# Optimization experiments

Measured on AMD Instinct MI355X. Metric: run time of the kernel, lower is better.

## Reference

```python
import jax, jax.numpy as jnp
import numpy as np

HIDDEN = 1024
INTER = 4096
NUM_EXPERTS = 8
TOP_K = 2


def setup_inputs() -> dict:
    key = jax.random.key(0)
    ks = jax.random.split(key, 6)
    B, S = 4, 2048
    hidden_states = jax.random.normal(ks[0], (B, S, HIDDEN), dtype=jnp.float32)
    scale = 0.02
    # nn.Linear stores weight as [out, in]; y = x @ W.T + b
    gate_w = jax.random.normal(ks[1], (NUM_EXPERTS, HIDDEN), dtype=jnp.float32) * scale
    W1 = jax.random.normal(ks[2], (NUM_EXPERTS, INTER, HIDDEN), dtype=jnp.float32) * scale
    b1 = jax.random.normal(ks[3], (NUM_EXPERTS, INTER), dtype=jnp.float32) * scale
    W2 = jax.random.normal(ks[4], (NUM_EXPERTS, HIDDEN, INTER), dtype=jnp.float32) * scale
    b2 = jax.random.normal(ks[5], (NUM_EXPERTS, HIDDEN), dtype=jnp.float32) * scale
    return {"hidden_states": hidden_states, "gate_w": gate_w,
            "W1": W1, "b1": b1, "W2": W2, "b2": b2}


def reference(hidden_states, gate_w, W1, b1, W2, b2):
    B, S, H = hidden_states.shape
    x = hidden_states.reshape(-1, H)                      # [T, H]
    # Gating: top-k logits -> softmax over the k selected experts only
    gate_logits = x @ gate_w.T                            # [T, E]
    top_vals, top_idx = jax.lax.top_k(gate_logits, TOP_K) # [T, K]
    weights = jax.nn.softmax(top_vals, axis=-1)           # [T, K]
    # Per-token combine weight for each expert (0 if not selected)
    one_hot = jax.nn.one_hot(top_idx, NUM_EXPERTS, dtype=x.dtype)  # [T, K, E]
    combine = jnp.einsum("tk,tke->te", weights, one_hot)           # [T, E]
    # Expert MLPs: fixed small loop over experts (structurally distinct params)
    out = jnp.zeros_like(x)
    for e in range(NUM_EXPERTS):
        h = jax.nn.gelu(x @ W1[e].T + b1[e], approximate=False)  # [T, INTER]
        y = h @ W2[e].T + b2[e]                                   # [T, H]
        out = out + combine[:, e:e + 1] * y
    return out.reshape(B, S, H)
```

## Files before the change

### kernel.cpp

```cpp
#include <hip/hip_runtime.h>
#include <hip/hip_bf16.h>
#include <stdint.h>

#define HID 1024
#define INTER_ 4096
#define NE 8
#define NTOK 8192
#define NPAIR (NTOK * 2)
#define MAXT 72

using f32x4 = __attribute__((ext_vector_type(4))) float;
using bf16x8 = __attribute__((ext_vector_type(8))) __bf16;
using ushort8v = __attribute__((ext_vector_type(8))) unsigned short;

__device__ __forceinline__ unsigned short f2b(float f) {
  unsigned int u = __float_as_uint(f);
  u += 0x7fffu + ((u >> 16) & 1u);
  return (unsigned short)(u >> 16);
}
__device__ __forceinline__ float b2f(unsigned short u) {
  return __uint_as_float((unsigned int)u << 16);
}

__device__ __forceinline__ float gelu_f(float v) {
  float z = fabsf(v) * 0.70710678118654752f;
  float t = __builtin_amdgcn_rcpf(1.f + 0.3275911f * z);
  float p = t * (0.254829592f +
            t * (-0.284496736f +
            t * (1.421413741f +
            t * (-1.453152027f + t * 1.061405429f))));
  float er = 1.f - p * __expf(-z * z);
  er = copysignf(er, v);
  return 0.5f * v * (1.f + er);
}

#define GLD_LDS(gp, lp)                                                        \
  __builtin_amdgcn_global_load_lds(                                            \
      (const __attribute__((address_space(1))) unsigned int*)(const void*)(gp),\
      (__attribute__((address_space(3))) unsigned int*)(void*)(lp), 16, 0, 0)

#define WAITV(N) asm volatile("s_waitcnt vmcnt(" #N ")" ::: "memory")

__global__ __launch_bounds__(256) void gate_kernel(
    const float* __restrict__ x, const float* __restrict__ gw,
    int* __restrict__ topi, float* __restrict__ topw,
    unsigned short* __restrict__ xb)
{
  int gwave = (blockIdx.x * 256 + threadIdx.x) >> 6;
  int lane = threadIdx.x & 63;
  if (gwave >= NTOK) return;
  const float* xr = x + (size_t)gwave * HID;
  unsigned short* xo = xb + (size_t)gwave * HID;
  float acc[NE];
#pragma unroll
  for (int e = 0; e < NE; ++e) acc[e] = 0.f;
#pragma unroll
  for (int q = 0; q < 4; ++q) {
    float4 v = *reinterpret_cast<const float4*>(xr + q * 256 + lane * 4);
    ushort4 uv;
    uv.x = f2b(v.x); uv.y = f2b(v.y); uv.z = f2b(v.z); uv.w = f2b(v.w);
    *reinterpret_cast<ushort4*>(xo + q * 256 + lane * 4) = uv;
#pragma unroll
    for (int e = 0; e < NE; ++e) {
      float4 wv = *reinterpret_cast<const float4*>(gw + e * HID + q * 256 + lane * 4);
      acc[e] += v.x * wv.x + v.y * wv.y + v.z * wv.z + v.w * wv.w;
    }
  }
#pragma unroll
  for (int e = 0; e < NE; ++e) {
#pragma unroll
    for (int off = 32; off > 0; off >>= 1) acc[e] += __shfl_xor(acc[e], off);
  }
  if (lane == 0) {
    float v0 = -1e30f; int i0 = 0;
#pragma unroll
    for (int e = 0; e < NE; ++e) if (acc[e] > v0) { v0 = acc[e]; i0 = e; }
    float v1 = -1e30f; int i1 = 0;
#pragma unroll
    for (int e = 0; e < NE; ++e) if (e != i0 && acc[e] > v1) { v1 = acc[e]; i1 = e; }
    float e1 = __expf(v1 - v0);
    float s = 1.f + e1;
    topi[gwave * 2] = i0; topi[gwave * 2 + 1] = i1;
    topw[gwave * 2] = 1.f / s; topw[gwave * 2 + 1] = e1 / s;
  }
}

__global__ __launch_bounds__(256) void hist_kernel(const int* __restrict__ topi,
                                                   int* __restrict__ bcnt)
{
  int tid = threadIdx.x, blk = blockIdx.x;
  int t = blk * 256 + tid;
  int e0 = topi[t * 2], e1 = topi[t * 2 + 1];
  int w = tid >> 6, lane = tid & 63;
  __shared__ int wcnt[4][NE];
#pragma unroll
  for (int e = 0; e < NE; ++e) {
    unsigned long long m0 = __ballot(e0 == e);
    unsigned long long m1 = __ballot(e1 == e);
    if (lane == 0) wcnt[w][e] = __popcll(m0) + __popcll(m1);
  }
  __syncthreads();
  if (tid < NE) {
    int s = 0;
#pragma unroll
    for (int w2 = 0; w2 < 4; ++w2) s += wcnt[w2][tid];
    bcnt[blk * NE + tid] = s;
  }
}

__global__ void scan2_kernel(const int* __restrict__ bcnt, int* __restrict__ offs,
                             int* __restrict__ tile_e, int* __restrict__ tile_m,
                             int* __restrict__ ntile, int* __restrict__ gbase)
{
  __shared__ int cnts[NE];
  __shared__ int soffs[NE];
  int tid = threadIdx.x;
  if (tid < NE) {
    int s = 0;
#pragma unroll
    for (int b = 0; b < 32; ++b) s += bcnt[b * NE + tid];
    cnts[tid] = s;
  }
  __syncthreads();
  if (tid == 0) {
    int o = 0, tt = 0;
    for (int e = 0; e < NE; ++e) {
      offs[e] = o; soffs[e] = o;
      int c = cnts[e];
      for (int m = 0; m < c; m += 256) { tile_e[tt] = e; tile_m[tt] = m; ++tt; }
      o += c;
    }
    offs[NE] = o;
    *ntile = tt;
  }
  __syncthreads();
  if (tid < 32 * NE) {
    int b = tid >> 3, e = tid & 7;
    int g = soffs[e];
    for (int b2 = 0; b2 < b; ++b2) g += bcnt[b2 * NE + e];
    gbase[b * NE + e] = g;
  }
}

__global__ __launch_bounds__(256) void scatter2_kernel(
    const int* __restrict__ topi, const float* __restrict__ topw,
    const int* __restrict__ gbase,
    int* __restrict__ toklist, float* __restrict__ wlist, int* __restrict__ pos)
{
  int tid = threadIdx.x, blk = blockIdx.x;
  int t = blk * 256 + tid;
  int e0 = topi[t * 2], e1 = topi[t * 2 + 1];
  float w0 = topw[t * 2], w1 = topw[t * 2 + 1];
  int w = tid >> 6, lane = tid & 63;
  unsigned long long lt = (1ull << lane) - 1ull;
  unsigned long long le = lt | (1ull << lane);
  __shared__ int wcnt[4][NE];
  __shared__ int wbase[4][NE];
  int r0 = 0, r1 = 0;
#pragma unroll
  for (int e = 0; e < NE; ++e) {
    unsigned long long m0 = __ballot(e0 == e);
    unsigned long long m1 = __ballot(e1 == e);
    if (lane == 0) wcnt[w][e] = __popcll(m0) + __popcll(m1);
    if (e0 == e) r0 = __popcll(m0 & lt) + __popcll(m1 & lt);
    if (e1 == e) r1 = __popcll(m0 & le) + __popcll(m1 & lt);
  }
  __syncthreads();
  if (tid < 4 * NE) {
    int w2 = tid >> 3, e = tid & 7;
    int b = gbase[blk * NE + e];
    for (int w3 = 0; w3 < w2; ++w3) b += wcnt[w3][e];
    wbase[w2][e] = b;
  }
  __syncthreads();
  int P0 = wbase[w][e0] + r0;
  int P1 = wbase[w][e1] + r1;
  toklist[P0] = t; wlist[P0] = w0; pos[t * 2] = P0;
  toklist[P1] = t; wlist[P1] = w1; pos[t * 2 + 1] = P1;
}

__global__ __launch_bounds__(256) void cvtw_kernel(
    const float* __restrict__ W1, const float* __restrict__ W2,
    unsigned short* __restrict__ w1b, unsigned short* __restrict__ w2b, int n8)
{
  int half = gridDim.x >> 1;
  const float* src = (blockIdx.x < half) ? W1 : W2;
  unsigned short* dst = (blockIdx.x < half) ? w1b : w2b;
  int b0 = (blockIdx.x < half) ? blockIdx.x : blockIdx.x - half;
  int stride = half * 256;
  for (int i = b0 * 256 + threadIdx.x; i < n8; i += stride) {
    const float4* s = reinterpret_cast<const float4*>(src) + (size_t)i * 2;
    float4 a = s[0], b = s[1];
    ushort8v u;
    u[0] = f2b(a.x); u[1] = f2b(a.y); u[2] = f2b(a.z); u[3] = f2b(a.w);
    u[4] = f2b(b.x); u[5] = f2b(b.y); u[6] = f2b(b.z); u[7] = f2b(b.w);
    reinterpret_cast<ushort8v*>(dst)[i] = u;
  }
}


__global__ __launch_bounds__(512, 2) void gemm1_kernel(
    const unsigned short* __restrict__ xb, const unsigned short* __restrict__ w1b,
    const float* __restrict__ b1,
    const int* __restrict__ toklist, const int* __restrict__ offs,
    const int* __restrict__ tile_e, const int* __restrict__ tile_m,
    const int* __restrict__ ntile,
    unsigned short* __restrict__ hb)
{
  const int t = blockIdx.y;
  if (t >= *ntile) return;
  const int e = tile_e[t];
  const int m0 = tile_m[t];
  const int base = offs[e];
  const int cnt = offs[e + 1] - base;
  const int n0 = blockIdx.x * 256;

  __shared__ __align__(16) unsigned short As[4][256 * 32];
  __shared__ __align__(16) unsigned short Bs[4][256 * 32];

  const int tid = threadIdx.x;
  const int lane = tid & 63;
  const int w = tid >> 6;
  const int wr = w >> 2, wc = w & 3;

  const int r0 = tid >> 2;
  const int sl = tid & 3;
  const int scg = sl ^ ((r0 >> 1) & 3);
  const unsigned short* gA[2];
  const unsigned short* gB[2];
#pragma unroll
  for (int g = 0; g < 2; ++g) {
    int row = g * 128 + r0;
    int mrow = m0 + row; if (mrow >= cnt) mrow = cnt - 1;
    int tk = toklist[base + mrow];
    gA[g] = xb + (size_t)tk * HID + scg * 8;
    gB[g] = w1b + ((size_t)e * INTER_ + n0 + row) * HID + scg * 8;
  }

  int raq[8], rbq[4];
#pragma unroll
  for (int i = 0; i < 8; ++i) {
    int rA = wr * 128 + i * 16 + (lane & 15);
    raq[i] = rA * 32 + (((lane >> 4) ^ ((rA >> 1) & 3)) * 8);
  }
#pragma unroll
  for (int j = 0; j < 4; ++j) {
    int rB = wc * 64 + j * 16 + (lane & 15);
    rbq[j] = rB * 32 + (((lane >> 4) ^ ((rB >> 1) & 3)) * 8);
  }

  f32x4 acc[8][4];
#pragma unroll
  for (int i = 0; i < 8; ++i)
#pragma unroll
    for (int j = 0; j < 4; ++j) acc[i][j] = (f32x4){0.f, 0.f, 0.f, 0.f};

  auto stage = [&](int s) {
    const int kof = s * 32;
    unsigned short* Ad = &As[s & 3][0];
    unsigned short* Bd = &Bs[s & 3][0];
#pragma unroll
    for (int g = 0; g < 2; ++g) {
      GLD_LDS(gA[g] + kof, Ad + g * 4096 + tid * 8);
      GLD_LDS(gB[g] + kof, Bd + g * 4096 + tid * 8);
    }
  };
  auto compute = [&](int s) {
    const unsigned short* Ab = &As[s & 3][0];
    const unsigned short* Bb = &Bs[s & 3][0];
    bf16x8 bfr[4];
#pragma unroll
    for (int j = 0; j < 4; ++j) bfr[j] = *reinterpret_cast<const bf16x8*>(Bb + rbq[j]);
#pragma unroll
    for (int i = 0; i < 8; ++i) {
      bf16x8 af = *reinterpret_cast<const bf16x8*>(Ab + raq[i]);
#pragma unroll
      for (int j = 0; j < 4; ++j)
        acc[i][j] = __builtin_amdgcn_mfma_f32_16x16x32_bf16(af, bfr[j], acc[i][j], 0, 0, 0);
    }
  };

  const int NS = HID / 32;
  stage(0); stage(1); stage(2);
#pragma unroll 4
  for (int s = 0; s < NS - 3; ++s) {
    WAITV(8);
    __builtin_amdgcn_s_barrier();
    stage(s + 3);
    compute(s);
  }
  WAITV(8); __builtin_amdgcn_s_barrier(); compute(NS - 3);
  WAITV(4); __builtin_amdgcn_s_barrier(); compute(NS - 2);
  WAITV(0); __builtin_amdgcn_s_barrier(); compute(NS - 1);

  float bias[4];
  const int colb = n0 + wc * 64 + (lane & 15);
#pragma unroll
  for (int j = 0; j < 4; ++j) bias[j] = b1[(size_t)e * INTER_ + colb + j * 16];
#pragma unroll
  for (int i = 0; i < 8; ++i) {
    int mbase = m0 + wr * 128 + i * 16 + (lane >> 4) * 4;
#pragma unroll
    for (int r = 0; r < 4; ++r) {
      int m = mbase + r;
      if (m < cnt) {
        unsigned short* hrow = hb + (size_t)(base + m) * INTER_ + colb;
#pragma unroll
        for (int j = 0; j < 4; ++j)
          hrow[j * 16] = f2b(gelu_f(acc[i][j][r] + bias[j]));
      }
    }
  }
}

__global__ __launch_bounds__(512, 2) void gemm2_kernel(
    const unsigned short* __restrict__ hb, const unsigned short* __restrict__ w2b,
    const int* __restrict__ offs,
    const int* __restrict__ tile_e, const int* __restrict__ tile_m,
    const int* __restrict__ ntile,
    unsigned short* __restrict__ part)
{
  const int t = blockIdx.y;
  if (t >= *ntile) return;
  const int e = tile_e[t];
  const int m0 = tile_m[t];
  const int base = offs[e];
  const int cnt = offs[e + 1] - base;
  const int n0 = blockIdx.x * 256;
  const int kbase = blockIdx.z * (INTER_ / 2);

  __shared__ __align__(16) unsigned short As[4][256 * 32];
  __shared__ __align__(16) unsigned short Bs[4][256 * 32];

  const int tid = threadIdx.x;
  const int lane = tid & 63;
  const int w = tid >> 6;
  const int wr = w >> 2, wc = w & 3;

  const int r0 = tid >> 2;
  const int sl = tid & 3;
  const int scg = sl ^ ((r0 >> 1) & 3);
  const unsigned short* gA[2];
  const unsigned short* gB[2];
#pragma unroll
  for (int g = 0; g < 2; ++g) {
    int row = g * 128 + r0;
    int mrow = m0 + row; if (mrow >= cnt) mrow = cnt - 1;
    gA[g] = hb + (size_t)(base + mrow) * INTER_ + kbase + scg * 8;
    gB[g] = w2b + ((size_t)e * HID + n0 + row) * INTER_ + kbase + scg * 8;
  }

  int raq[8], rbq[4];
#pragma unroll
  for (int i = 0; i < 8; ++i) {
    int rA = wr * 128 + i * 16 + (lane & 15);
    raq[i] = rA * 32 + (((lane >> 4) ^ ((rA >> 1) & 3)) * 8);
  }
#pragma unroll
  for (int j = 0; j < 4; ++j) {
    int rB = wc * 64 + j * 16 + (lane & 15);
    rbq[j] = rB * 32 + (((lane >> 4) ^ ((rB >> 1) & 3)) * 8);
  }

  f32x4 acc[8][4];
#pragma unroll
  for (int i = 0; i < 8; ++i)
#pragma unroll
    for (int j = 0; j < 4; ++j) acc[i][j] = (f32x4){0.f, 0.f, 0.f, 0.f};

  auto stage = [&](int s) {
    const int kof = s * 32;
    unsigned short* Ad = &As[s & 3][0];
    unsigned short* Bd = &Bs[s & 3][0];
#pragma unroll
    for (int g = 0; g < 2; ++g) {
      GLD_LDS(gA[g] + kof, Ad + g * 4096 + tid * 8);
      GLD_LDS(gB[g] + kof, Bd + g * 4096 + tid * 8);
    }
  };
  auto compute = [&](int s) {
    const unsigned short* Ab = &As[s & 3][0];
    const unsigned short* Bb = &Bs[s & 3][0];
    bf16x8 bfr[4];
#pragma unroll
    for (int j = 0; j < 4; ++j) bfr[j] = *reinterpret_cast<const bf16x8*>(Bb + rbq[j]);
#pragma unroll
    for (int i = 0; i < 8; ++i) {
      bf16x8 af = *reinterpret_cast<const bf16x8*>(Ab + raq[i]);
#pragma unroll
      for (int j = 0; j < 4; ++j)
        acc[i][j] = __builtin_amdgcn_mfma_f32_16x16x32_bf16(af, bfr[j], acc[i][j], 0, 0, 0);
    }
  };

  const int NS = (INTER_ / 2) / 32;
  stage(0); stage(1); stage(2);
#pragma unroll 4
  for (int s = 0; s < NS - 3; ++s) {
    WAITV(8);
    __builtin_amdgcn_s_barrier();
    stage(s + 3);
    compute(s);
  }
  WAITV(8); __builtin_amdgcn_s_barrier(); compute(NS - 3);
  WAITV(4); __builtin_amdgcn_s_barrier(); compute(NS - 2);
  WAITV(0); __builtin_amdgcn_s_barrier(); compute(NS - 1);

  const int colb = n0 + wc * 64 + (lane & 15);
  unsigned short* pbase = part + (size_t)blockIdx.z * NPAIR * HID;
#pragma unroll
  for (int i = 0; i < 8; ++i) {
    int mbase = m0 + wr * 128 + i * 16 + (lane >> 4) * 4;
#pragma unroll
    for (int r = 0; r < 4; ++r) {
      int m = mbase + r;
      if (m < cnt) {
        unsigned short* prow = pbase + (size_t)(base + m) * HID + colb;
#pragma unroll
        for (int j = 0; j < 4; ++j)
          prow[j * 16] = f2b(acc[i][j][r]);
      }
    }
  }
}

__global__ __launch_bounds__(256) void combine_kernel(
    const unsigned short* __restrict__ part, const float* __restrict__ b2,
    const int* __restrict__ topi, const float* __restrict__ topw,
    const int* __restrict__ pos, float* __restrict__ out)
{
  int t = blockIdx.x * 4 + (threadIdx.x >> 6);
  int lane = threadIdx.x & 63;
  int c0 = lane * 16;
  float o[16];
#pragma unroll
  for (int c = 0; c < 16; ++c) o[c] = 0.f;
#pragma unroll
  for (int k = 0; k < 2; ++k) {
    int p = pos[t * 2 + k];
    int e = topi[t * 2 + k];
    float wk = topw[t * 2 + k];
    const unsigned short* rp0 = part + (size_t)p * HID + c0;
    const unsigned short* rp1 = part + ((size_t)NPAIR + p) * HID + c0;
    const float* bb = b2 + (size_t)e * HID + c0;
#pragma unroll
    for (int v = 0; v < 2; ++v) {
      ushort8v a = *reinterpret_cast<const ushort8v*>(rp0 + v * 8);
      ushort8v b = *reinterpret_cast<const ushort8v*>(rp1 + v * 8);
      float4 bb0 = *reinterpret_cast<const float4*>(bb + v * 8);
      float4 bb1 = *reinterpret_cast<const float4*>(bb + v * 8 + 4);
      o[v * 8 + 0] += wk * (b2f(a[0]) + b2f(b[0]) + bb0.x);
      o[v * 8 + 1] += wk * (b2f(a[1]) + b2f(b[1]) + bb0.y);
      o[v * 8 + 2] += wk * (b2f(a[2]) + b2f(b[2]) + bb0.z);
      o[v * 8 + 3] += wk * (b2f(a[3]) + b2f(b[3]) + bb0.w);
      o[v * 8 + 4] += wk * (b2f(a[4]) + b2f(b[4]) + bb1.x);
      o[v * 8 + 5] += wk * (b2f(a[5]) + b2f(b[5]) + bb1.y);
      o[v * 8 + 6] += wk * (b2f(a[6]) + b2f(b[6]) + bb1.z);
      o[v * 8 + 7] += wk * (b2f(a[7]) + b2f(b[7]) + bb1.w);
    }
  }
  float4* op = reinterpret_cast<float4*>(out + (size_t)t * HID + c0);
#pragma unroll
  for (int v = 0; v < 4; ++v)
    op[v] = make_float4(o[v * 4], o[v * 4 + 1], o[v * 4 + 2], o[v * 4 + 3]);
}

extern "C" void kernel_launch(void* const* d_in, const int* in_sizes, int n_in,
                              void* d_out, int out_size, void* d_ws, size_t ws_size,
                              hipStream_t stream) {
  const float* x  = (const float*)d_in[0];
  const float* gw = (const float*)d_in[1];
  const float* W1 = (const float*)d_in[2];
  const float* b1 = (const float*)d_in[3];
  const float* W2 = (const float*)d_in[4];
  const float* b2 = (const float*)d_in[5];
  float* out = (float*)d_out;

  char* ws = (char*)d_ws;
  size_t off = 0;
  auto alloc = [&](size_t bytes) -> void* {
    void* p = ws + off;
    off += (bytes + 255) & ~(size_t)255;
    return p;
  };
  unsigned short* hb   = (unsigned short*)alloc((size_t)NPAIR * INTER_ * 2);
  unsigned short* xb   = (unsigned short*)alloc((size_t)NTOK * HID * 2);
  unsigned short* w1b  = (unsigned short*)alloc((size_t)NE * INTER_ * HID * 2);
  unsigned short* w2b  = (unsigned short*)alloc((size_t)NE * HID * INTER_ * 2);
  unsigned short* part = (unsigned short*)alloc((size_t)2 * NPAIR * HID * 2);
  int*   toklist = (int*)alloc(NPAIR * 4);
  float* wlist   = (float*)alloc(NPAIR * 4);
  int*   topi    = (int*)alloc(NTOK * 2 * 4);
  float* topw    = (float*)alloc(NTOK * 2 * 4);
  int*   pos     = (int*)alloc(NTOK * 2 * 4);
  int*   bcnt    = (int*)alloc(32 * NE * 4);
  int*   gbase   = (int*)alloc(32 * NE * 4);
  int*   offs    = (int*)alloc(64);
  int*   tile_e  = (int*)alloc(MAXT * 4);
  int*   tile_m  = (int*)alloc(MAXT * 4);
  int*   ntile   = (int*)alloc(64);

  gate_kernel<<<NTOK / 4, 256, 0, stream>>>(x, gw, topi, topw, xb);
  hist_kernel<<<32, 256, 0, stream>>>(topi, bcnt);
  scan2_kernel<<<1, 256, 0, stream>>>(bcnt, offs, tile_e, tile_m, ntile, gbase);
  scatter2_kernel<<<32, 256, 0, stream>>>(topi, topw, gbase, toklist, wlist, pos);
  cvtw_kernel<<<4096, 256, 0, stream>>>(W1, W2, w1b, w2b, NE * INTER_ * HID / 8);
  gemm1_kernel<<<dim3(INTER_ / 256, MAXT), 512, 0, stream>>>(
      xb, w1b, b1, toklist, offs, tile_e, tile_m, ntile, hb);
  gemm2_kernel<<<dim3(HID / 256, MAXT, 2), 512, 0, stream>>>(
      hb, w2b, offs, tile_e, tile_m, ntile, part);
  combine_kernel<<<NTOK / 4, 256, 0, stream>>>(part, b2, topi, topw, pos, out);
}
```

Before: 548.4 us.

## Drop split-K in second expert GEMM and batch LDS fragment loads with MFMA priority

The second GEMM no longer splits the K dimension across two z-blocks. Each block now covers the full INTER reduction and writes a single partial buffer, so the combine kernel reads one bf16 row instead of two and the extra partial rounding goes away. In both GEMMs the compute step now loads A fragments in two batches of four, waits on LDS, and issues the MFMAs under raised wave priority with scheduling barriers. The cost is that gemm2 launches half as many blocks, which can lower occupancy when few tiles are active, and the explicit lgkmcnt waits may serialize LDS reads against MFMA work.

```diff
diff --git a/kernel.cpp b/kernel.cpp
--- a/kernel.cpp
+++ b/kernel.cpp
@@ -40,6 +40,8 @@
       (__attribute__((address_space(3))) unsigned int*)(void*)(lp), 16, 0, 0)
 
 #define WAITV(N) asm volatile("s_waitcnt vmcnt(" #N ")" ::: "memory")
+#define WAITL0   asm volatile("s_waitcnt lgkmcnt(0)" ::: "memory")
+#define SBAR     __builtin_amdgcn_sched_barrier(0)
 
 __global__ __launch_bounds__(256) void gate_kernel(
     const float* __restrict__ x, const float* __restrict__ gw,
@@ -268,16 +270,32 @@
   auto compute = [&](int s) {
     const unsigned short* Ab = &As[s & 3][0];
     const unsigned short* Bb = &Bs[s & 3][0];
-    bf16x8 bfr[4];
+    bf16x8 bfr[4], afr[4];
 #pragma unroll
     for (int j = 0; j < 4; ++j) bfr[j] = *reinterpret_cast<const bf16x8*>(Bb + rbq[j]);
 #pragma unroll
-    for (int i = 0; i < 8; ++i) {
-      bf16x8 af = *reinterpret_cast<const bf16x8*>(Ab + raq[i]);
+    for (int i = 0; i < 4; ++i) afr[i] = *reinterpret_cast<const bf16x8*>(Ab + raq[i]);
+    WAITL0; SBAR;
+    __builtin_amdgcn_s_setprio(1);
+#pragma unroll
+    for (int i = 0; i < 4; ++i)
 #pragma unroll
       for (int j = 0; j < 4; ++j)
-        acc[i][j] = __builtin_amdgcn_mfma_f32_16x16x32_bf16(af, bfr[j], acc[i][j], 0, 0, 0);
-    }
+        acc[i][j] = __builtin_amdgcn_mfma_f32_16x16x32_bf16(afr[i], bfr[j], acc[i][j], 0, 0, 0);
+    __builtin_amdgcn_s_setprio(0);
+    SBAR;
+    bf16x8 afr2[4];
+#pragma unroll
+    for (int i = 0; i < 4; ++i) afr2[i] = *reinterpret_cast<const bf16x8*>(Ab + raq[4 + i]);
+    WAITL0; SBAR;
+    __builtin_amdgcn_s_setprio(1);
+#pragma unroll
+    for (int i = 0; i < 4; ++i)
+#pragma unroll
+      for (int j = 0; j < 4; ++j)
+        acc[4 + i][j] = __builtin_amdgcn_mfma_f32_16x16x32_bf16(afr2[i], bfr[j], acc[4 + i][j], 0, 0, 0);
+    __builtin_amdgcn_s_setprio(0);
+    SBAR;
   };
 
   const int NS = HID / 32;
@@ -327,7 +345,6 @@
   const int base = offs[e];
   const int cnt = offs[e + 1] - base;
   const int n0 = blockIdx.x * 256;
-  const int kbase = blockIdx.z * (INTER_ / 2);
 
   __shared__ __align__(16) unsigned short As[4][256 * 32];
   __shared__ __align__(16) unsigned short Bs[4][256 * 32];
@@ -346,8 +363,8 @@
   for (int g = 0; g < 2; ++g) {
     int row = g * 128 + r0;
     int mrow = m0 + row; if (mrow >= cnt) mrow = cnt - 1;
-    gA[g] = hb + (size_t)(base + mrow) * INTER_ + kbase + scg * 8;
-    gB[g] = w2b + ((size_t)e * HID + n0 + row) * INTER_ + kbase + scg * 8;
+    gA[g] = hb + (size_t)(base + mrow) * INTER_ + scg * 8;
+    gB[g] = w2b + ((size_t)e * HID + n0 + row) * INTER_ + scg * 8;
   }
 
   int raq[8], rbq[4];
@@ -381,19 +398,35 @@
   auto compute = [&](int s) {
     const unsigned short* Ab = &As[s & 3][0];
     const unsigned short* Bb = &Bs[s & 3][0];
-    bf16x8 bfr[4];
+    bf16x8 bfr[4], afr[4];
 #pragma unroll
     for (int j = 0; j < 4; ++j) bfr[j] = *reinterpret_cast<const bf16x8*>(Bb + rbq[j]);
 #pragma unroll
-    for (int i = 0; i < 8; ++i) {
-      bf16x8 af = *reinterpret_cast<const bf16x8*>(Ab + raq[i]);
+    for (int i = 0; i < 4; ++i) afr[i] = *reinterpret_cast<const bf16x8*>(Ab + raq[i]);
+    WAITL0; SBAR;
+    __builtin_amdgcn_s_setprio(1);
+#pragma unroll
+    for (int i = 0; i < 4; ++i)
 #pragma unroll
       for (int j = 0; j < 4; ++j)
-        acc[i][j] = __builtin_amdgcn_mfma_f32_16x16x32_bf16(af, bfr[j], acc[i][j], 0, 0, 0);
-    }
+        acc[i][j] = __builtin_amdgcn_mfma_f32_16x16x32_bf16(afr[i], bfr[j], acc[i][j], 0, 0, 0);
+    __builtin_amdgcn_s_setprio(0);
+    SBAR;
+    bf16x8 afr2[4];
+#pragma unroll
+    for (int i = 0; i < 4; ++i) afr2[i] = *reinterpret_cast<const bf16x8*>(Ab + raq[4 + i]);
+    WAITL0; SBAR;
+    __builtin_amdgcn_s_setprio(1);
+#pragma unroll
+    for (int i = 0; i < 4; ++i)
+#pragma unroll
+      for (int j = 0; j < 4; ++j)
+        acc[4 + i][j] = __builtin_amdgcn_mfma_f32_16x16x32_bf16(afr2[i], bfr[j], acc[4 + i][j], 0, 0, 0);
+    __builtin_amdgcn_s_setprio(0);
+    SBAR;
   };
 
-  const int NS = (INTER_ / 2) / 32;
+  const int NS = INTER_ / 32;
   stage(0); stage(1); stage(2);
 #pragma unroll 4
   for (int s = 0; s < NS - 3; ++s) {
@@ -407,7 +440,6 @@
   WAITV(0); __builtin_amdgcn_s_barrier(); compute(NS - 1);
 
   const int colb = n0 + wc * 64 + (lane & 15);
-  unsigned short* pbase = part + (size_t)blockIdx.z * NPAIR * HID;
 #pragma unroll
   for (int i = 0; i < 8; ++i) {
     int mbase = m0 + wr * 128 + i * 16 + (lane >> 4) * 4;
@@ -415,7 +447,7 @@
     for (int r = 0; r < 4; ++r) {
       int m = mbase + r;
       if (m < cnt) {
-        unsigned short* prow = pbase + (size_t)(base + m) * HID + colb;
+        unsigned short* prow = part + (size_t)(base + m) * HID + colb;
 #pragma unroll
         for (int j = 0; j < 4; ++j)
           prow[j * 16] = f2b(acc[i][j][r]);
@@ -440,23 +472,21 @@
     int p = pos[t * 2 + k];
     int e = topi[t * 2 + k];
     float wk = topw[t * 2 + k];
-    const unsigned short* rp0 = part + (size_t)p * HID + c0;
-    const unsigned short* rp1 = part + ((size_t)NPAIR + p) * HID + c0;
+    const unsigned short* rp = part + (size_t)p * HID + c0;
     const float* bb = b2 + (size_t)e * HID + c0;
 #pragma unroll
     for (int v = 0; v < 2; ++v) {
-      ushort8v a = *reinterpret_cast<const ushort8v*>(rp0 + v * 8);
-      ushort8v b = *reinterpret_cast<const ushort8v*>(rp1 + v * 8);
+      ushort8v a = *reinterpret_cast<const ushort8v*>(rp + v * 8);
       float4 bb0 = *reinterpret_cast<const float4*>(bb + v * 8);
       float4 bb1 = *reinterpret_cast<const float4*>(bb + v * 8 + 4);
-      o[v * 8 + 0] += wk * (b2f(a[0]) + b2f(b[0]) + bb0.x);
-      o[v * 8 + 1] += wk * (b2f(a[1]) + b2f(b[1]) + bb0.y);
-      o[v * 8 + 2] += wk * (b2f(a[2]) + b2f(b[2]) + bb0.z);
-      o[v * 8 + 3] += wk * (b2f(a[3]) + b2f(b[3]) + bb0.w);
-      o[v * 8 + 4] += wk * (b2f(a[4]) + b2f(b[4]) + bb1.x);
-      o[v * 8 + 5] += wk * (b2f(a[5]) + b2f(b[5]) + bb1.y);
-      o[v * 8 + 6] += wk * (b2f(a[6]) + b2f(b[6]) + bb1.z);
-      o[v * 8 + 7] += wk * (b2f(a[7]) + b2f(b[7]) + bb1.w);
+      o[v * 8 + 0] += wk * (b2f(a[0]) + bb0.x);
+      o[v * 8 + 1] += wk * (b2f(a[1]) + bb0.y);
+      o[v * 8 + 2] += wk * (b2f(a[2]) + bb0.z);
+      o[v * 8 + 3] += wk * (b2f(a[3]) + bb0.w);
+      o[v * 8 + 4] += wk * (b2f(a[4]) + bb1.x);
+      o[v * 8 + 5] += wk * (b2f(a[5]) + bb1.y);
+      o[v * 8 + 6] += wk * (b2f(a[6]) + bb1.z);
+      o[v * 8 + 7] += wk * (b2f(a[7]) + bb1.w);
     }
   }
   float4* op = reinterpret_cast<float4*>(out + (size_t)t * HID + c0);
@@ -487,7 +517,7 @@
   unsigned short* xb   = (unsigned short*)alloc((size_t)NTOK * HID * 2);
   unsigned short* w1b  = (unsigned short*)alloc((size_t)NE * INTER_ * HID * 2);
   unsigned short* w2b  = (unsigned short*)alloc((size_t)NE * HID * INTER_ * 2);
-  unsigned short* part = (unsigned short*)alloc((size_t)2 * NPAIR * HID * 2);
+  unsigned short* part = (unsigned short*)alloc((size_t)NPAIR * HID * 2);
   int*   toklist = (int*)alloc(NPAIR * 4);
   float* wlist   = (float*)alloc(NPAIR * 4);
   int*   topi    = (int*)alloc(NTOK * 2 * 4);
@@ -507,7 +537,7 @@
   cvtw_kernel<<<4096, 256, 0, stream>>>(W1, W2, w1b, w2b, NE * INTER_ * HID / 8);
   gemm1_kernel<<<dim3(INTER_ / 256, MAXT), 512, 0, stream>>>(
       xb, w1b, b1, toklist, offs, tile_e, tile_m, ntile, hb);
-  gemm2_kernel<<<dim3(HID / 256, MAXT, 2), 512, 0, stream>>>(
+  gemm2_kernel<<<dim3(HID / 256, MAXT), 512, 0, stream>>>(
       hb, w2b, offs, tile_e, tile_m, ntile, part);
   combine_kernel<<<NTOK / 4, 256, 0, stream>>>(part, b2, topi, topw, pos, out);
 }
```

Measured after the change: 682.3 us. 24.4% more time.

## Shrink GEMM tiles to 256x128 with 3-stage pipeline for higher occupancy

Applied to the files above, without the earlier changes.

Both expert GEMM kernels now compute 256x128 output tiles instead of 256x256, with eight waves arranged 4x2 and each wave holding a 64x64 accumulator block. The LDS pipeline drops from four to three stages, the B tile is halved, and launch bounds now target four blocks per CU. The grid doubles along N. The aim is to cut register and LDS use per block so more blocks can be resident and latency is better hidden. The cost is lower arithmetic intensity per block, since each A tile is reloaded for twice as many N tiles, and a shallower prefetch depth.

```diff
diff --git a/kernel.cpp b/kernel.cpp
--- a/kernel.cpp
+++ b/kernel.cpp
@@ -199,7 +199,7 @@
 }
 
 
-__global__ __launch_bounds__(512, 2) void gemm1_kernel(
+__global__ __launch_bounds__(512, 4) void gemm1_kernel(
     const unsigned short* __restrict__ xb, const unsigned short* __restrict__ w1b,
     const float* __restrict__ b1,
     const int* __restrict__ toklist, const int* __restrict__ offs,
@@ -213,66 +213,59 @@
   const int m0 = tile_m[t];
   const int base = offs[e];
   const int cnt = offs[e + 1] - base;
-  const int n0 = blockIdx.x * 256;
-
-  __shared__ __align__(16) unsigned short As[4][256 * 32];
-  __shared__ __align__(16) unsigned short Bs[4][256 * 32];
+  const int n0 = blockIdx.x * 128;
+
+  __shared__ __align__(16) unsigned short As[3][256 * 32];
+  __shared__ __align__(16) unsigned short Bs[3][128 * 32];
 
   const int tid = threadIdx.x;
   const int lane = tid & 63;
   const int w = tid >> 6;
-  const int wr = w >> 2, wc = w & 3;
+  const int wr = w >> 1, wc = w & 1;
 
   const int r0 = tid >> 2;
   const int sl = tid & 3;
   const int scg = sl ^ ((r0 >> 1) & 3);
   const unsigned short* gA[2];
-  const unsigned short* gB[2];
+  const unsigned short* gB;
 #pragma unroll
   for (int g = 0; g < 2; ++g) {
     int row = g * 128 + r0;
     int mrow = m0 + row; if (mrow >= cnt) mrow = cnt - 1;
     int tk = toklist[base + mrow];
     gA[g] = xb + (size_t)tk * HID + scg * 8;
-    gB[g] = w1b + ((size_t)e * INTER_ + n0 + row) * HID + scg * 8;
-  }
-
-  int raq[8], rbq[4];
-#pragma unroll
-  for (int i = 0; i < 8; ++i) {
-    int rA = wr * 128 + i * 16 + (lane & 15);
+  }
+  gB = w1b + ((size_t)e * INTER_ + n0 + r0) * HID + scg * 8;
+
+  int raq[4], rbq[4];
+#pragma unroll
+  for (int i = 0; i < 4; ++i) {
+    int rA = wr * 64 + i * 16 + (lane & 15);
     raq[i] = rA * 32 + (((lane >> 4) ^ ((rA >> 1) & 3)) * 8);
-  }
-#pragma unroll
-  for (int j = 0; j < 4; ++j) {
-    int rB = wc * 64 + j * 16 + (lane & 15);
-    rbq[j] = rB * 32 + (((lane >> 4) ^ ((rB >> 1) & 3)) * 8);
-  }
-
-  f32x4 acc[8][4];
-#pragma unroll
-  for (int i = 0; i < 8; ++i)
+    int rB = wc * 64 + i * 16 + (lane & 15);
+    rbq[i] = rB * 32 + (((lane >> 4) ^ ((rB >> 1) & 3)) * 8);
+  }
+
+  f32x4 acc[4][4];
+#pragma unroll
+  for (int i = 0; i < 4; ++i)
 #pragma unroll
     for (int j = 0; j < 4; ++j) acc[i][j] = (f32x4){0.f, 0.f, 0.f, 0.f};
 
-  auto stage = [&](int s) {
+  auto stage = [&](int slot, int s) {
     const int kof = s * 32;
-    unsigned short* Ad = &As[s & 3][0];
-    unsigned short* Bd = &Bs[s & 3][0];
-#pragma unroll
-    for (int g = 0; g < 2; ++g) {
-      GLD_LDS(gA[g] + kof, Ad + g * 4096 + tid * 8);
-      GLD_LDS(gB[g] + kof, Bd + g * 4096 + tid * 8);
-    }
+    GLD_LDS(gA[0] + kof, &As[slot][tid * 8]);
+    GLD_LDS(gA[1] + kof, &As[slot][4096 + tid * 8]);
+    GLD_LDS(gB + kof,    &Bs[slot][tid * 8]);
   };
-  auto compute = [&](int s) {
-    const unsigned short* Ab = &As[s & 3][0];
-    const unsigned short* Bb = &Bs[s & 3][0];
+  auto compute = [&](int slot) {
+    const unsigned short* Ab = &As[slot][0];
+    const unsigned short* Bb = &Bs[slot][0];
     bf16x8 bfr[4];
 #pragma unroll
     for (int j = 0; j < 4; ++j) bfr[j] = *reinterpret_cast<const bf16x8*>(Bb + rbq[j]);
 #pragma unroll
-    for (int i = 0; i < 8; ++i) {
+    for (int i = 0; i < 4; ++i) {
       bf16x8 af = *reinterpret_cast<const bf16x8*>(Ab + raq[i]);
 #pragma unroll
       for (int j = 0; j < 4; ++j)
@@ -281,25 +274,24 @@
   };
 
   const int NS = HID / 32;
-  stage(0); stage(1); stage(2);
-#pragma unroll 4
-  for (int s = 0; s < NS - 3; ++s) {
-    WAITV(8);
+  stage(0, 0); stage(1, 1);
+#pragma unroll 3
+  for (int s = 0; s < NS - 2; ++s) {
+    WAITV(3);
     __builtin_amdgcn_s_barrier();
-    stage(s + 3);
-    compute(s);
-  }
-  WAITV(8); __builtin_amdgcn_s_barrier(); compute(NS - 3);
-  WAITV(4); __builtin_amdgcn_s_barrier(); compute(NS - 2);
-  WAITV(0); __builtin_amdgcn_s_barrier(); compute(NS - 1);
+    stage((s + 2) % 3, s + 2);
+    compute(s % 3);
+  }
+  WAITV(3); __builtin_amdgcn_s_barrier(); compute((NS - 2) % 3);
+  WAITV(0); __builtin_amdgcn_s_barrier(); compute((NS - 1) % 3);
 
   float bias[4];
   const int colb = n0 + wc * 64 + (lane & 15);
 #pragma unroll
   for (int j = 0; j < 4; ++j) bias[j] = b1[(size_t)e * INTER_ + colb + j * 16];
 #pragma unroll
-  for (int i = 0; i < 8; ++i) {
-    int mbase = m0 + wr * 128 + i * 16 + (lane >> 4) * 4;
+  for (int i = 0; i < 4; ++i) {
+    int mbase = m0 + wr * 64 + i * 16 + (lane >> 4) * 4;
 #pragma unroll
     for (int r = 0; r < 4; ++r) {
       int m = mbase + r;
@@ -313,7 +305,7 @@
   }
 }
 
-__global__ __launch_bounds__(512, 2) void gemm2_kernel(
+__global__ __launch_bounds__(512, 4) void gemm2_kernel(
     const unsigned short* __restrict__ hb, const unsigned short* __restrict__ w2b,
     const int* __restrict__ offs,
     const int* __restrict__ tile_e, const int* __restrict__ tile_m,
@@ -326,66 +318,59 @@
   const int m0 = tile_m[t];
   const int base = offs[e];
   const int cnt = offs[e + 1] - base;
-  const int n0 = blockIdx.x * 256;
+  const int n0 = blockIdx.x * 128;
   const int kbase = blockIdx.z * (INTER_ / 2);
 
-  __shared__ __align__(16) unsigned short As[4][256 * 32];
-  __shared__ __align__(16) unsigned short Bs[4][256 * 32];
+  __shared__ __align__(16) unsigned short As[3][256 * 32];
+  __shared__ __align__(16) unsigned short Bs[3][128 * 32];
 
   const int tid = threadIdx.x;
   const int lane = tid & 63;
   const int w = tid >> 6;
-  const int wr = w >> 2, wc = w & 3;
+  const int wr = w >> 1, wc = w & 1;
 
   const int r0 = tid >> 2;
   const int sl = tid & 3;
   const int scg = sl ^ ((r0 >> 1) & 3);
   const unsigned short* gA[2];
-  const unsigned short* gB[2];
+  const unsigned short* gB;
 #pragma unroll
   for (int g = 0; g < 2; ++g) {
     int row = g * 128 + r0;
     int mrow = m0 + row; if (mrow >= cnt) mrow = cnt - 1;
     gA[g] = hb + (size_t)(base + mrow) * INTER_ + kbase + scg * 8;
-    gB[g] = w2b + ((size_t)e * HID + n0 + row) * INTER_ + kbase + scg * 8;
-  }
-
-  int raq[8], rbq[4];
-#pragma unroll
-  for (int i = 0; i < 8; ++i) {
-    int rA = wr * 128 + i * 16 + (lane & 15);
+  }
+  gB = w2b + ((size_t)e * HID + n0 + r0) * INTER_ + kbase + scg * 8;
+
+  int raq[4], rbq[4];
+#pragma unroll
+  for (int i = 0; i < 4; ++i) {
+    int rA = wr * 64 + i * 16 + (lane & 15);
     raq[i] = rA * 32 + (((lane >> 4) ^ ((rA >> 1) & 3)) * 8);
-  }
-#pragma unroll
-  for (int j = 0; j < 4; ++j) {
-    int rB = wc * 64 + j * 16 + (lane & 15);
-    rbq[j] = rB * 32 + (((lane >> 4) ^ ((rB >> 1) & 3)) * 8);
-  }
-
-  f32x4 acc[8][4];
-#pragma unroll
-  for (int i = 0; i < 8; ++i)
+    int rB = wc * 64 + i * 16 + (lane & 15);
+    rbq[i] = rB * 32 + (((lane >> 4) ^ ((rB >> 1) & 3)) * 8);
+  }
+
+  f32x4 acc[4][4];
+#pragma unroll
+  for (int i = 0; i < 4; ++i)
 #pragma unroll
     for (int j = 0; j < 4; ++j) acc[i][j] = (f32x4){0.f, 0.f, 0.f, 0.f};
 
-  auto stage = [&](int s) {
+  auto stage = [&](int slot, int s) {
     const int kof = s * 32;
-    unsigned short* Ad = &As[s & 3][0];
-    unsigned short* Bd = &Bs[s & 3][0];
-#pragma unroll
-    for (int g = 0; g < 2; ++g) {
-      GLD_LDS(gA[g] + kof, Ad + g * 4096 + tid * 8);
-      GLD_LDS(gB[g] + kof, Bd + g * 4096 + tid * 8);
-    }
+    GLD_LDS(gA[0] + kof, &As[slot][tid * 8]);
+    GLD_LDS(gA[1] + kof, &As[slot][4096 + tid * 8]);
+    GLD_LDS(gB + kof,    &Bs[slot][tid * 8]);
   };
-  auto compute = [&](int s) {
-    const unsigned short* Ab = &As[s & 3][0];
-    const unsigned short* Bb = &Bs[s & 3][0];
+  auto compute = [&](int slot) {
+    const unsigned short* Ab = &As[slot][0];
+    const unsigned short* Bb = &Bs[slot][0];
     bf16x8 bfr[4];
 #pragma unroll
     for (int j = 0; j < 4; ++j) bfr[j] = *reinterpret_cast<const bf16x8*>(Bb + rbq[j]);
 #pragma unroll
-    for (int i = 0; i < 8; ++i) {
+    for (int i = 0; i < 4; ++i) {
       bf16x8 af = *reinterpret_cast<const bf16x8*>(Ab + raq[i]);
 #pragma unroll
       for (int j = 0; j < 4; ++j)
@@ -394,23 +379,22 @@
   };
 
   const int NS = (INTER_ / 2) / 32;
-  stage(0); stage(1); stage(2);
-#pragma unroll 4
-  for (int s = 0; s < NS - 3; ++s) {
-    WAITV(8);
+  stage(0, 0); stage(1, 1);
+#pragma unroll 3
+  for (int s = 0; s < NS - 2; ++s) {
+    WAITV(3);
     __builtin_amdgcn_s_barrier();
-    stage(s + 3);
-    compute(s);
-  }
-  WAITV(8); __builtin_amdgcn_s_barrier(); compute(NS - 3);
-  WAITV(4); __builtin_amdgcn_s_barrier(); compute(NS - 2);
-  WAITV(0); __builtin_amdgcn_s_barrier(); compute(NS - 1);
+    stage((s + 2) % 3, s + 2);
+    compute(s % 3);
+  }
+  WAITV(3); __builtin_amdgcn_s_barrier(); compute((NS - 2) % 3);
+  WAITV(0); __builtin_amdgcn_s_barrier(); compute((NS - 1) % 3);
 
   const int colb = n0 + wc * 64 + (lane & 15);
   unsigned short* pbase = part + (size_t)blockIdx.z * NPAIR * HID;
 #pragma unroll
-  for (int i = 0; i < 8; ++i) {
-    int mbase = m0 + wr * 128 + i * 16 + (lane >> 4) * 4;
+  for (int i = 0; i < 4; ++i) {
+    int mbase = m0 + wr * 64 + i * 16 + (lane >> 4) * 4;
 #pragma unroll
     for (int r = 0; r < 4; ++r) {
       int m = mbase + r;
@@ -505,9 +489,9 @@
   scan2_kernel<<<1, 256, 0, stream>>>(bcnt, offs, tile_e, tile_m, ntile, gbase);
   scatter2_kernel<<<32, 256, 0, stream>>>(topi, topw, gbase, toklist, wlist, pos);
   cvtw_kernel<<<4096, 256, 0, stream>>>(W1, W2, w1b, w2b, NE * INTER_ * HID / 8);
-  gemm1_kernel<<<dim3(INTER_ / 256, MAXT), 512, 0, stream>>>(
+  gemm1_kernel<<<dim3(INTER_ / 128, MAXT), 512, 0, stream>>>(
       xb, w1b, b1, toklist, offs, tile_e, tile_m, ntile, hb);
-  gemm2_kernel<<<dim3(HID / 256, MAXT, 2), 512, 0, stream>>>(
+  gemm2_kernel<<<dim3(HID / 128, MAXT, 2), 512, 0, stream>>>(
       hb, w2b, offs, tile_e, tile_m, ntile, part);
   combine_kernel<<<NTOK / 4, 256, 0, stream>>>(part, b2, topi, topw, pos, out);
 }
```

Measured after the change: 533.7 us. -2.7%, faster.
